# Kernel optimization log

Measured on AMD Instinct MI355X. Metric: run time of the kernel, lower is better.

Reference implementation:

```python
import jax, jax.numpy as jnp
import numpy as np

N_NODES = 40000
N_EDGES = 640000
D = 128
EPS = 1e-12  # F.normalize clamp_min eps


def setup_inputs() -> dict:
    key = jax.random.key(0)
    ks = jax.random.split(key, 8)
    scale = 1.0 / np.sqrt(D)
    return {
        "x": jax.random.normal(ks[0], (N_NODES, D), dtype=jnp.float32),
        "edge_index": jax.random.randint(ks[1], (2, N_EDGES), 0, N_NODES, dtype=jnp.int64),
        "W_l0": jax.random.normal(ks[2], (D, D), dtype=jnp.float32) * scale,
        "b_l0": jnp.zeros((D,), dtype=jnp.float32),
        "W_r0": jax.random.normal(ks[3], (D, D), dtype=jnp.float32) * scale,
        "W_l1": jax.random.normal(ks[4], (D, D), dtype=jnp.float32) * scale,
        "b_l1": jnp.zeros((D,), dtype=jnp.float32),
        "W_r1": jax.random.normal(ks[5], (D, D), dtype=jnp.float32) * scale,
    }


def _sage_conv(x, src, dst, W_l, b_l, W_r):
    # mean-aggregate neighbor features: messages flow src -> dst (PyG convention)
    msg = x[src]  # [E, D] gather
    summed = jax.ops.segment_sum(msg, dst, num_segments=N_NODES)  # [N, D]
    cnt = jax.ops.segment_sum(jnp.ones_like(dst, dtype=x.dtype), dst, num_segments=N_NODES)
    agg = summed / jnp.maximum(cnt, 1.0)[:, None]
    out = agg @ W_l + b_l + x @ W_r  # lin_l(agg) + lin_r(x)
    # normalize=True -> L2 normalize along feature dim
    norm = jnp.linalg.norm(out, axis=-1, keepdims=True)
    return out / jnp.maximum(norm, EPS)


def reference(x, edge_index, W_l0, b_l0, W_r0, W_l1, b_l1, W_r1):
    src, dst = edge_index[0], edge_index[1]
    h = jax.nn.relu(_sage_conv(x, src, dst, W_l0, b_l0, W_r0))  # layer 0 + relu
    h = _sage_conv(h, src, dst, W_l1, b_l1, W_r1)  # last layer, no relu
    return h
```

## Files before the change

### kernel.cpp

```cpp
#include <hip/hip_runtime.h>

#define DF 128
#define EPSN 1e-12f
#define SL 48
#define CAP 6144

typedef __attribute__((ext_vector_type(8))) short short8;
typedef __attribute__((ext_vector_type(8))) unsigned short ushort8;
typedef __attribute__((ext_vector_type(4))) float float4v;

__device__ inline unsigned short f2bf(float f) {
    unsigned u = __builtin_bit_cast(unsigned, f);
    u += 0x7fffu + ((u >> 16) & 1u);
    return (unsigned short)(u >> 16);
}
__device__ inline float bf2f(unsigned short h) {
    unsigned u = ((unsigned)h) << 16;
    return __builtin_bit_cast(float, u);
}


__global__ __launch_bounds__(256) void prep_kernel(const int* __restrict__ src,
                                                   const int* __restrict__ dst,
                                                   unsigned* __restrict__ gcur,
                                                   unsigned* __restrict__ buf, int E,
                                                   const float* __restrict__ x,
                                                   unsigned short* __restrict__ xb,
                                                   unsigned char* __restrict__ xq,
                                                   unsigned char* __restrict__ hq,
                                                   const float* __restrict__ Wl0,
                                                   const float* __restrict__ Wr0,
                                                   const float* __restrict__ Wl1,
                                                   const float* __restrict__ Wr1,
                                                   unsigned short* __restrict__ Wp,
                                                   int n, int nb, int eb, int qb) {
    int b = blockIdx.x, t = threadIdx.x;
    if (b < eb) {
        __shared__ int lcnt[160];
        __shared__ int lbase[160];
        if (t < nb) lcnt[t] = 0;
        __syncthreads();
        int e0 = b * 1024;
        int bk[4], pp[4];
        unsigned rec[4];
#pragma unroll
        for (int k = 0; k < 4; ++k) {
            int e = e0 + k * 256 + t;
            if (e < E) {
                int d = dst[e];
                int s = src[e];
                bk[k] = d >> 8;
                rec[k] = ((unsigned)(d & 255) << 16) | (unsigned)s;
                pp[k] = atomicAdd(&lcnt[bk[k]], 1);
            } else {
                bk[k] = -1; pp[k] = 0; rec[k] = 0;
            }
        }
        __syncthreads();
        if (t < nb) {
            int c = lcnt[t];
            lbase[t] = (c > 0) ? (int)atomicAdd(&gcur[t], (unsigned)c) : 0;
        }
        __syncthreads();
#pragma unroll
        for (int k = 0; k < 4; ++k) {
            if (bk[k] >= 0) {
                int p = lbase[bk[k]] + pp[k];
                if (p < CAP) buf[(size_t)bk[k] * CAP + p] = rec[k];
            }
        }
    } else if (b < eb + qb) {
        int r = (b - eb) * 4 + (t >> 6);
        int lane = t & 63;
        if (r >= n) return;
        float2 v = ((const float2*)(x + (size_t)r * DF))[lane];
        unsigned h0 = f2bf(v.x), h1 = f2bf(v.y);
        ((unsigned*)xb)[(size_t)r * 64 + lane] = h0 | (h1 << 16);
        const float qs = 127.f / 6.f;
        int q0 = (int)rintf(fminf(fmaxf(v.x, -6.f), 6.f) * qs) + 128;
        int q1 = (int)rintf(fminf(fmaxf(v.y, -6.f), 6.f) * qs) + 128;
        ((unsigned short*)xq)[(size_t)r * 64 + lane] = (unsigned short)(q0 | (q1 << 8));
    } else {
        int i = (b - eb - qb) * 256 + t;
        if (i >= 8192) return;
        if (i < DF) {
            xq[(size_t)n * DF + i] = 128;
            hq[(size_t)n * DF + i] = 0;
        }
        int layer = i >> 12;
        int t2 = i & 4095;
        int nt = t2 >> 9;
        int kk = (t2 >> 6) & 7;
        int lane = t2 & 63;
        int g = lane >> 4, c = lane & 15;
        const float* Wl = layer ? Wl1 : Wl0;
        const float* Wr = layer ? Wr1 : Wr0;
        ushort8 o;
#pragma unroll
        for (int j = 0; j < 8; ++j) {
            int k = kk * 32 + g * 8 + j;
            int ncol = nt * 16 + c;
            float v = (k < 128) ? Wl[k * 128 + ncol] : Wr[(k - 128) * 128 + ncol];
            o[j] = f2bf(v);
        }
        ((ushort8*)Wp)[i] = o;
    }
}


__global__ __launch_bounds__(256) void ellfill_kernel(const unsigned* __restrict__ gcur,
                                                      const unsigned* __restrict__ buf,
                                                      unsigned short* __restrict__ ell,
                                                      int* __restrict__ cnt, int n) {
    __shared__ unsigned short lell[256 * SL];
    __shared__ int lcnt[256];
    int b = blockIdx.x, t = threadIdx.x;
    lcnt[t] = 0;
    __syncthreads();
    int ne = (int)gcur[b];
    if (ne > CAP) ne = CAP;
    const unsigned* ebuf = buf + (size_t)b * CAP;
    int i = t;
    for (; i + 768 < ne; i += 1024) {
        unsigned r0 = ebuf[i], r1 = ebuf[i + 256], r2 = ebuf[i + 512], r3 = ebuf[i + 768];
        int d0 = r0 >> 16, d1 = r1 >> 16, d2 = r2 >> 16, d3 = r3 >> 16;
        int p0 = atomicAdd(&lcnt[d0], 1);
        if (p0 < SL) lell[d0 * SL + p0] = (unsigned short)r0;
        int p1 = atomicAdd(&lcnt[d1], 1);
        if (p1 < SL) lell[d1 * SL + p1] = (unsigned short)r1;
        int p2 = atomicAdd(&lcnt[d2], 1);
        if (p2 < SL) lell[d2 * SL + p2] = (unsigned short)r2;
        int p3 = atomicAdd(&lcnt[d3], 1);
        if (p3 < SL) lell[d3 * SL + p3] = (unsigned short)r3;
    }
    for (; i < ne; i += 256) {
        unsigned r = ebuf[i];
        int d = r >> 16;
        int p = atomicAdd(&lcnt[d], 1);
        if (p < SL) lell[d * SL + p] = (unsigned short)r;
    }
    __syncthreads();
    const unsigned* ldw = (const unsigned*)lell;
    unsigned* gdw = (unsigned*)(ell + (size_t)b * 256 * SL);
    for (int j = t; j < 256 * SL / 2; j += 256) gdw[j] = ldw[j];
    int node = b * 256 + t;
    if (node < n) cnt[node] = lcnt[t];
}


template <int MODE>
__global__ __launch_bounds__(256, 4) void layer_kernel(const unsigned char* __restrict__ tabq,
                                                       const int* __restrict__ cnt,
                                                       const unsigned short* __restrict__ ell,
                                                       const unsigned short* __restrict__ A1,
                                                       const unsigned short* __restrict__ Wp,
                                                       const float* __restrict__ bias,
                                                       void* __restrict__ outv,
                                                       unsigned char* __restrict__ hq,
                                                       int n) {
    constexpr float TSCALE = (MODE == 0) ? (6.f / 127.f) : (1.f / 255.f);
    constexpr int TBIAS = (MODE == 0) ? 128 : 0;
    constexpr int SMW = (MODE == 0) ? (64 * 136 / 2) : (64 * 136);
    __shared__ float smbuf[SMW];
    unsigned short* la = (unsigned short*)smbuf;
    int tid = threadIdx.x;
    int wid = tid >> 6;
    int lane = tid & 63;
    int q = lane >> 4, c = lane & 15;
    int wrow = blockIdx.x * 64 + wid * 16;
    const uint2* rq = (const uint2*)tabq;

    for (int i2 = 0; i2 < 8; ++i2) {
        int mA = wrow + i2 * 2;
        int mB = mA + 1;
        int mAc = (mA < n) ? mA : (n - 1);
        int mBc = (mB < n) ? mB : (n - 1);
        int degA = cnt[mAc], degB = cnt[mBc];
        int limA = (degA < SL) ? degA : SL;
        int limB = (degB < SL) ? degB : SL;
        const unsigned short* rA = ell + (size_t)mAc * SL;
        const unsigned short* rB = ell + (size_t)mBc * SL;

        unsigned pA[4] = {0u, 0u, 0u, 0u};
        unsigned pB[4] = {0u, 0u, 0u, 0u};

        int s = 0;
        do {
            int ia[4], ib[4];
#pragma unroll
            for (int t4 = 0; t4 < 4; ++t4) {
                int pos = s + t4 * 4 + q;
                int vA = rA[pos];
                int vB = rB[pos];
                ia[t4] = (pos < limA) ? vA : n;
                ib[t4] = (pos < limB) ? vB : n;
            }
            uint2 va[4], vb[4];
#pragma unroll
            for (int t4 = 0; t4 < 4; ++t4) {
                va[t4] = rq[(size_t)ia[t4] * 16 + c];
                vb[t4] = rq[(size_t)ib[t4] * 16 + c];
            }
#pragma unroll
            for (int t4 = 0; t4 < 4; ++t4) {
                unsigned a0 = va[t4].x, a1 = va[t4].y;
                unsigned b0 = vb[t4].x, b1 = vb[t4].y;
                pA[0] += a0 & 0x00FF00FFu;
                pA[1] += (a0 >> 8) & 0x00FF00FFu;
                pA[2] += a1 & 0x00FF00FFu;
                pA[3] += (a1 >> 8) & 0x00FF00FFu;
                pB[0] += b0 & 0x00FF00FFu;
                pB[1] += (b0 >> 8) & 0x00FF00FFu;
                pB[2] += b1 & 0x00FF00FFu;
                pB[3] += (b1 >> 8) & 0x00FF00FFu;
            }
            s += 16;
        } while (s < limA || s < limB);

#pragma unroll
        for (int d = 0; d < 4; ++d) {
            pA[d] += (unsigned)__shfl_xor((int)pA[d], 16);
            pA[d] += (unsigned)__shfl_xor((int)pA[d], 32);
            pB[d] += (unsigned)__shfl_xor((int)pB[d], 16);
            pB[d] += (unsigned)__shfl_xor((int)pB[d], 32);
        }
        if (q == 0) {
            float corr = (float)(TBIAS * s);
            float invA = TSCALE / fmaxf((float)degA, 1.0f);
            float invB = TSCALE / fmaxf((float)degB, 1.0f);
            ushort8 oA, oB;
            oA[0] = f2bf(((float)(pA[0] & 0xFFFFu) - corr) * invA);
            oA[1] = f2bf(((float)(pA[1] & 0xFFFFu) - corr) * invA);
            oA[2] = f2bf(((float)(pA[0] >> 16) - corr) * invA);
            oA[3] = f2bf(((float)(pA[1] >> 16) - corr) * invA);
            oA[4] = f2bf(((float)(pA[2] & 0xFFFFu) - corr) * invA);
            oA[5] = f2bf(((float)(pA[3] & 0xFFFFu) - corr) * invA);
            oA[6] = f2bf(((float)(pA[2] >> 16) - corr) * invA);
            oA[7] = f2bf(((float)(pA[3] >> 16) - corr) * invA);
            oB[0] = f2bf(((float)(pB[0] & 0xFFFFu) - corr) * invB);
            oB[1] = f2bf(((float)(pB[1] & 0xFFFFu) - corr) * invB);
            oB[2] = f2bf(((float)(pB[0] >> 16) - corr) * invB);
            oB[3] = f2bf(((float)(pB[1] >> 16) - corr) * invB);
            oB[4] = f2bf(((float)(pB[2] & 0xFFFFu) - corr) * invB);
            oB[5] = f2bf(((float)(pB[3] & 0xFFFFu) - corr) * invB);
            oB[6] = f2bf(((float)(pB[2] >> 16) - corr) * invB);
            oB[7] = f2bf(((float)(pB[3] >> 16) - corr) * invB);
            *(ushort8*)&la[(wid * 16 + i2 * 2) * 136 + c * 8] = oA;
            *(ushort8*)&la[(wid * 16 + i2 * 2 + 1) * 136 + c * 8] = oB;
        }
    }
    __syncthreads();

    int row = wrow + c;
    int rowc = (row < n) ? row : (n - 1);
    float4v acc[8];
#pragma unroll
    for (int nt = 0; nt < 8; ++nt) acc[nt] = (float4v){0.f, 0.f, 0.f, 0.f};

    const short8* wp8 = (const short8*)Wp;
#pragma unroll
    for (int kk = 0; kk < 8; ++kk) {
        short8 a;
        if (kk < 4) a = *(const short8*)&la[(wid * 16 + c) * 136 + kk * 32 + q * 8];
        else a = *(const short8*)(A1 + (size_t)rowc * DF + (kk - 4) * 32 + q * 8);
#pragma unroll
        for (int nt = 0; nt < 8; ++nt) {
            short8 bfr = wp8[(nt * 8 + kk) * 64 + lane];
            acc[nt] = __builtin_amdgcn_mfma_f32_16x16x32_bf16(a, bfr, acc[nt], 0, 0, 0);
        }
    }
    __syncthreads();

    float val[8][4];
    float ss[4] = {0.f, 0.f, 0.f, 0.f};
#pragma unroll
    for (int nt = 0; nt < 8; ++nt) {
        float b = bias[nt * 16 + c];
#pragma unroll
        for (int r = 0; r < 4; ++r) {
            float v = acc[nt][r] + b;
            val[nt][r] = v;
            ss[r] += v * v;
        }
    }
#pragma unroll
    for (int r = 0; r < 4; ++r) {
        float v = ss[r];
        v += __shfl_xor(v, 1);
        v += __shfl_xor(v, 2);
        v += __shfl_xor(v, 4);
        v += __shfl_xor(v, 8);
        ss[r] = v;
    }
    float invs[4];
#pragma unroll
    for (int r = 0; r < 4; ++r) invs[r] = 1.0f / fmaxf(sqrtf(ss[r]), EPSN);

    if (MODE == 0) {
#pragma unroll
        for (int nt = 0; nt < 8; ++nt) {
#pragma unroll
            for (int r = 0; r < 4; ++r) {
                float v = fmaxf(val[nt][r] * invs[r], 0.f);
                la[(wid * 16 + q * 4 + r) * 136 + nt * 16 + c] = f2bf(v);
            }
        }
        __syncthreads();
        unsigned short* out = (unsigned short*)outv;
#pragma unroll
        for (int it = 0; it < 4; ++it) {
            int r = it * 4 + q;
            int m = wrow + r;
            ushort8 o = *(const ushort8*)&la[(wid * 16 + r) * 136 + c * 8];
            unsigned u0 = 0, u1 = 0;
#pragma unroll
            for (int j = 0; j < 4; ++j) {
                u0 |= ((unsigned)(unsigned char)(int)rintf(bf2f(o[j]) * 255.f) << (8 * j));
                u1 |= ((unsigned)(unsigned char)(int)rintf(bf2f(o[4 + j]) * 255.f) << (8 * j));
            }
            if (m < n) {
                *(ushort8*)(out + (size_t)m * DF + c * 8) = o;
                *(uint2*)(hq + (size_t)m * DF + c * 8) = make_uint2(u0, u1);
            }
        }
    } else {
#pragma unroll
        for (int nt = 0; nt < 8; ++nt) {
#pragma unroll
            for (int r = 0; r < 4; ++r) {
                smbuf[(wid * 16 + q * 4 + r) * 136 + nt * 16 + c] = val[nt][r] * invs[r];
            }
        }
        __syncthreads();
        float* out = (float*)outv;
#pragma unroll
        for (int it = 0; it < 8; ++it) {
            int r = it * 2 + (lane >> 5);
            int cc = lane & 31;
            int m = wrow + r;
            float4v v = *(const float4v*)&smbuf[(wid * 16 + r) * 136 + cc * 4];
            if (m < n) *(float4v*)(out + (size_t)m * DF + cc * 4) = v;
        }
    }
}


extern "C" void kernel_launch(void* const* d_in, const int* in_sizes, int n_in,
                              void* d_out, int out_size, void* d_ws, size_t ws_size,
                              hipStream_t stream) {
    const float* x   = (const float*)d_in[0];
    const int*   ei  = (const int*)d_in[1];
    const float* Wl0 = (const float*)d_in[2];
    const float* bl0 = (const float*)d_in[3];
    const float* Wr0 = (const float*)d_in[4];
    const float* Wl1 = (const float*)d_in[5];
    const float* bl1 = (const float*)d_in[6];
    const float* Wr1 = (const float*)d_in[7];

    int N = in_sizes[0] / DF;
    int E = in_sizes[1] / 2;
    const int* src = ei;
    const int* dst = ei + E;

    int NB = (N + 255) >> 8;

    char* w = (char*)d_ws;
    auto alloc = [&](size_t bytes) {
        void* p = (void*)w;
        w += (bytes + 255) & ~(size_t)255;
        return p;
    };
    unsigned*       gcur = (unsigned*)alloc((size_t)NB * 4);
    unsigned*       buf  = (unsigned*)alloc((size_t)NB * CAP * 4);
    unsigned short* ell  = (unsigned short*)alloc((size_t)NB * 256 * SL * 2);
    int*            cnt  = (int*)alloc((size_t)N * 4);
    unsigned short* xb   = (unsigned short*)alloc((size_t)N * DF * 2);
    unsigned char*  xq   = (unsigned char*)alloc((size_t)(N + 1) * DF);
    unsigned short* hb   = (unsigned short*)alloc((size_t)N * DF * 2);
    unsigned char*  hq   = (unsigned char*)alloc((size_t)(N + 1) * DF);
    unsigned short* Wp   = (unsigned short*)alloc((size_t)2 * 4096 * 8 * 2);
    float* outf = (float*)d_out;

    int eb = (E + 1023) / 1024;
    int qb = (N + 3) / 4;

    hipMemsetAsync(gcur, 0, (size_t)NB * 4, stream);
    prep_kernel<<<eb + qb + 32, 256, 0, stream>>>(src, dst, gcur, buf, E,
                                                  x, xb, xq, hq,
                                                  Wl0, Wr0, Wl1, Wr1, Wp, N, NB, eb, qb);
    ellfill_kernel<<<NB, 256, 0, stream>>>(gcur, buf, ell, cnt, N);

    int LB = (N + 63) / 64;

    layer_kernel<0><<<LB, 256, 0, stream>>>(xq, cnt, ell, xb, Wp, bl0, hb, hq, N);
    layer_kernel<1><<<LB, 256, 0, stream>>>(hq, cnt, ell, hb, Wp + 32768, bl1, outf, hq, N);
}
```

Baseline: 108.1 us.

## Prefetch ELL indices across row pairs, drop bf16 hidden buffer, read uint8 self-features

The gather loop now loads each wave's degrees once and broadcasts them with shuffles. It also prefetches the first 16 neighbor indices of the next row pair while the current pair is being accumulated, which hides the index-load latency. Layer 0 no longer writes a bf16 copy of the hidden state. Layer 1 instead reads the uint8-quantized hidden rows and dequantizes them in registers for the self-term MFMA, which cuts global writes and reads. This adds register pressure, and the self-term becomes slightly less precise through quantization. The ELL buffer is padded so tail rows can be read without clamping.

```diff
diff --git a/kernel.cpp b/kernel.cpp
--- a/kernel.cpp
+++ b/kernel.cpp
@@ -152,7 +152,7 @@
 __global__ __launch_bounds__(256, 4) void layer_kernel(const unsigned char* __restrict__ tabq,
                                                        const int* __restrict__ cnt,
                                                        const unsigned short* __restrict__ ell,
-                                                       const unsigned short* __restrict__ A1,
+                                                       const void* __restrict__ A1,
                                                        const unsigned short* __restrict__ Wp,
                                                        const float* __restrict__ bias,
                                                        void* __restrict__ outv,
@@ -170,30 +170,52 @@
     int wrow = blockIdx.x * 64 + wid * 16;
     const uint2* rq = (const uint2*)tabq;
 
+    int r16 = wrow + (lane & 15);
+    int myDeg = cnt[(r16 < n) ? r16 : (n - 1)];
+
+    int nia[4], nib[4];
+    {
+        const unsigned short* rA0 = ell + (size_t)wrow * SL;
+#pragma unroll
+        for (int t4 = 0; t4 < 4; ++t4) {
+            int pos = t4 * 4 + q;
+            nia[t4] = rA0[pos];
+            nib[t4] = rA0[SL + pos];
+        }
+    }
+
+#pragma unroll
     for (int i2 = 0; i2 < 8; ++i2) {
-        int mA = wrow + i2 * 2;
-        int mB = mA + 1;
-        int mAc = (mA < n) ? mA : (n - 1);
-        int mBc = (mB < n) ? mB : (n - 1);
-        int degA = cnt[mAc], degB = cnt[mBc];
+        int degA = __shfl(myDeg, i2 * 2);
+        int degB = __shfl(myDeg, i2 * 2 + 1);
         int limA = (degA < SL) ? degA : SL;
         int limB = (degB < SL) ? degB : SL;
-        const unsigned short* rA = ell + (size_t)mAc * SL;
-        const unsigned short* rB = ell + (size_t)mBc * SL;
+        const unsigned short* rA = ell + (size_t)(wrow + i2 * 2) * SL;
+        const unsigned short* rB = rA + SL;
+
+        int cia[4], cib[4];
+#pragma unroll
+        for (int t4 = 0; t4 < 4; ++t4) { cia[t4] = nia[t4]; cib[t4] = nib[t4]; }
+        if (i2 < 7) {
+            const unsigned short* rA2 = rB + SL;
+#pragma unroll
+            for (int t4 = 0; t4 < 4; ++t4) {
+                int pos = t4 * 4 + q;
+                nia[t4] = rA2[pos];
+                nib[t4] = rA2[SL + pos];
+            }
+        }
 
         unsigned pA[4] = {0u, 0u, 0u, 0u};
         unsigned pB[4] = {0u, 0u, 0u, 0u};
 
-        int s = 0;
-        do {
+        {
             int ia[4], ib[4];
 #pragma unroll
             for (int t4 = 0; t4 < 4; ++t4) {
-                int pos = s + t4 * 4 + q;
-                int vA = rA[pos];
-                int vB = rB[pos];
-                ia[t4] = (pos < limA) ? vA : n;
-                ib[t4] = (pos < limB) ? vB : n;
+                int pos = t4 * 4 + q;
+                ia[t4] = (pos < limA) ? cia[t4] : n;
+                ib[t4] = (pos < limB) ? cib[t4] : n;
             }
             uint2 va[4], vb[4];
 #pragma unroll
@@ -214,8 +236,39 @@
                 pB[2] += b1 & 0x00FF00FFu;
                 pB[3] += (b1 >> 8) & 0x00FF00FFu;
             }
+        }
+        int s = 16;
+        while (s < limA || s < limB) {
+            int ia[4], ib[4];
+#pragma unroll
+            for (int t4 = 0; t4 < 4; ++t4) {
+                int pos = s + t4 * 4 + q;
+                int vA = rA[pos];
+                int vB = rB[pos];
+                ia[t4] = (pos < limA) ? vA : n;
+                ib[t4] = (pos < limB) ? vB : n;
+            }
+            uint2 va[4], vb[4];
+#pragma unroll
+            for (int t4 = 0; t4 < 4; ++t4) {
+                va[t4] = rq[(size_t)ia[t4] * 16 + c];
+                vb[t4] = rq[(size_t)ib[t4] * 16 + c];
+            }
+#pragma unroll
+            for (int t4 = 0; t4 < 4; ++t4) {
+                unsigned a0 = va[t4].x, a1 = va[t4].y;
+                unsigned b0 = vb[t4].x, b1 = vb[t4].y;
+                pA[0] += a0 & 0x00FF00FFu;
+                pA[1] += (a0 >> 8) & 0x00FF00FFu;
+                pA[2] += a1 & 0x00FF00FFu;
+                pA[3] += (a1 >> 8) & 0x00FF00FFu;
+                pB[0] += b0 & 0x00FF00FFu;
+                pB[1] += (b0 >> 8) & 0x00FF00FFu;
+                pB[2] += b1 & 0x00FF00FFu;
+                pB[3] += (b1 >> 8) & 0x00FF00FFu;
+            }
             s += 16;
-        } while (s < limA || s < limB);
+        }
 
 #pragma unroll
         for (int d = 0; d < 4; ++d) {
@@ -261,8 +314,19 @@
 #pragma unroll
     for (int kk = 0; kk < 8; ++kk) {
         short8 a;
-        if (kk < 4) a = *(const short8*)&la[(wid * 16 + c) * 136 + kk * 32 + q * 8];
-        else a = *(const short8*)(A1 + (size_t)rowc * DF + (kk - 4) * 32 + q * 8);
+        if (kk < 4) {
+            a = *(const short8*)&la[(wid * 16 + c) * 136 + kk * 32 + q * 8];
+        } else if (MODE == 0) {
+            a = *(const short8*)((const unsigned short*)A1 + (size_t)rowc * DF + (kk - 4) * 32 + q * 8);
+        } else {
+            uint2 qv = *(const uint2*)((const unsigned char*)A1 + (size_t)rowc * DF + (kk - 4) * 32 + q * 8);
+            const float s255 = 1.f / 255.f;
+#pragma unroll
+            for (int j = 0; j < 4; ++j) {
+                a[j] = (short)f2bf((float)((qv.x >> (8 * j)) & 0xffu) * s255);
+                a[4 + j] = (short)f2bf((float)((qv.y >> (8 * j)) & 0xffu) * s255);
+            }
+        }
 #pragma unroll
         for (int nt = 0; nt < 8; ++nt) {
             short8 bfr = wp8[(nt * 8 + kk) * 64 + lane];
@@ -306,7 +370,6 @@
             }
         }
         __syncthreads();
-        unsigned short* out = (unsigned short*)outv;
 #pragma unroll
         for (int it = 0; it < 4; ++it) {
             int r = it * 4 + q;
@@ -319,7 +382,6 @@
                 u1 |= ((unsigned)(unsigned char)(int)rintf(bf2f(o[4 + j]) * 255.f) << (8 * j));
             }
             if (m < n) {
-                *(ushort8*)(out + (size_t)m * DF + c * 8) = o;
                 *(uint2*)(hq + (size_t)m * DF + c * 8) = make_uint2(u0, u1);
             }
         }
@@ -372,11 +434,10 @@
     };
     unsigned*       gcur = (unsigned*)alloc((size_t)NB * 4);
     unsigned*       buf  = (unsigned*)alloc((size_t)NB * CAP * 4);
-    unsigned short* ell  = (unsigned short*)alloc((size_t)NB * 256 * SL * 2);
+    unsigned short* ell  = (unsigned short*)alloc(((size_t)NB * 256 * SL + 64) * 2);
     int*            cnt  = (int*)alloc((size_t)N * 4);
     unsigned short* xb   = (unsigned short*)alloc((size_t)N * DF * 2);
     unsigned char*  xq   = (unsigned char*)alloc((size_t)(N + 1) * DF);
-    unsigned short* hb   = (unsigned short*)alloc((size_t)N * DF * 2);
     unsigned char*  hq   = (unsigned char*)alloc((size_t)(N + 1) * DF);
     unsigned short* Wp   = (unsigned short*)alloc((size_t)2 * 4096 * 8 * 2);
     float* outf = (float*)d_out;
@@ -392,6 +453,6 @@
 
     int LB = (N + 63) / 64;
 
-    layer_kernel<0><<<LB, 256, 0, stream>>>(xq, cnt, ell, xb, Wp, bl0, hb, hq, N);
-    layer_kernel<1><<<LB, 256, 0, stream>>>(hq, cnt, ell, hb, Wp + 32768, bl1, outf, hq, N);
-}
+    layer_kernel<0><<<LB, 256, 0, stream>>>(xq, cnt, ell, xb, Wp, bl0, nullptr, hq, N);
+    layer_kernel<1><<<LB, 256, 0, stream>>>(hq, cnt, ell, hq, Wp + 32768, bl1, outf, hq, N);
+}
```

Result: faster. 97.18 us (median of 2 runs) (-10.1%).
